# Kernel optimization log

Hardware: AMD Instinct MI355X
Metric: run time of the kernel (lower is better)

The kernel has to match this reference:

```python
import jax, jax.numpy as jnp
import numpy as np

EPS = 1e-12
LORA_RANK = 16

def setup_inputs() -> dict:
    key = jax.random.key(0)
    ks = jax.random.split(key, 7)
    bs, sq, din, dout = 8, 2048, 2048, 2048
    n_tasks, n_splits, n_skills, r = 32, 1, 8, LORA_RANK
    return {
        'x': jax.random.normal(ks[0], (bs, sq, din), dtype=jnp.float32),
        'W': jax.random.normal(ks[1], (dout, din), dtype=jnp.float32) * (1.0 / np.sqrt(din)),
        'b': jax.random.normal(ks[2], (dout,), dtype=jnp.float32) * 0.02,
        'module_logits': jax.random.normal(ks[3], (n_tasks, n_splits * n_skills), dtype=jnp.float32) * 0.001,
        'A': jax.random.normal(ks[4], (n_splits, n_skills, din // n_splits, r), dtype=jnp.float32) * 0.02,
        'B': jax.random.normal(ks[5], (n_splits, n_skills, r, dout // n_splits), dtype=jnp.float32) * 0.02,
        'tasks': jax.random.randint(ks[6], (bs,), 0, n_tasks),
    }

def reference(x, W, b, module_logits, A, B, tasks):
    bs, sq, din = x.shape
    n_splits, n_skills, _, r = A.shape
    dout = W.shape[0]
    # Polytropon selector (eval mode): sigmoid + normalize over skills
    probs = jax.nn.sigmoid(module_logits[tasks]).reshape(bs, n_splits, n_skills)
    probs = probs / (probs.sum(-1, keepdims=True) + EPS)  # [bs, p, t]
    # WeightedSum combinor: per-example skill mixture of LoRA params
    A_c = jnp.einsum('bpt,ptir->bpir', probs, A)  # [bs, p, din/p, r]
    B_c = jnp.einsum('bpt,ptro->bpro', probs, B)  # [bs, p, r, dout/p]
    # LoRA forward: reshape to per-example [din, r] and [r, dout]
    A_r = A_c.reshape(bs, din, r)
    B_r = jnp.transpose(B_c, (0, 2, 1, 3)).reshape(bs, r, dout)
    lora = jnp.einsum('bsr,bro->bso', jnp.einsum('bsi,bir->bsr', x, A_r), B_r)
    base = jnp.einsum('bsi,oi->bso', x, W) + b
    return base + lora * (1.0 / r)
```

## Files before the change

### kernel.cpp

```cpp
#include <hip/hip_runtime.h>

typedef __attribute__((ext_vector_type(4))) float f32x4;
typedef __attribute__((ext_vector_type(8))) short bf16x8;

__device__ __forceinline__ unsigned short f2b(float f) {
  unsigned u = __float_as_uint(f);
  u = (u + 0x7FFFu + ((u >> 16) & 1u)) >> 16;
  return (unsigned short)u;
}

#define BAR() asm volatile("s_barrier" ::: "memory")
#define VMCNT(N) asm volatile("s_waitcnt vmcnt(" #N ")" ::: "memory")

__global__ void combine_kernel(const float* __restrict__ logits,
                               const int*   __restrict__ tasks,
                               const float* __restrict__ A,
                               const float* __restrict__ B,
                               unsigned short* __restrict__ Art,
                               unsigned short* __restrict__ Brt)
{
  int idx = blockIdx.x * 256 + threadIdx.x;
  int b = idx >> 11;
  int i = idx & 2047;
  if (b >= 8) return;
  int task = tasks[b];
  float p[8]; float s = 0.f;
  #pragma unroll
  for (int t = 0; t < 8; ++t) {
    float l = logits[task * 8 + t];
    float e = 1.f / (1.f + __expf(-l));
    p[t] = e; s += e;
  }
  float inv = 1.f / (s + 1e-12f);
  #pragma unroll
  for (int t = 0; t < 8; ++t) p[t] *= inv;

  float ar[16];
  #pragma unroll
  for (int r = 0; r < 16; ++r) ar[r] = 0.f;
  for (int t = 0; t < 8; ++t) {
    const float* ap = A + ((size_t)t * 2048 + i) * 16;
    float pt = p[t];
    #pragma unroll
    for (int r = 0; r < 16; ++r) ar[r] += pt * ap[r];
  }
  #pragma unroll
  for (int r = 0; r < 16; ++r)
    Art[((size_t)b * 16 + r) * 2048 + i] = f2b(ar[r]);

  float br[16];
  #pragma unroll
  for (int r = 0; r < 16; ++r) br[r] = 0.f;
  for (int t = 0; t < 8; ++t) {
    float pt = p[t];
    #pragma unroll
    for (int r = 0; r < 16; ++r) br[r] += pt * B[((size_t)t * 16 + r) * 2048 + i];
  }
  #pragma unroll
  for (int r = 0; r < 16; ++r)
    Brt[((size_t)b * 2048 + i) * 16 + r] = f2b(br[r] * 0.0625f);
}

__global__ void prep_kernel(const float* __restrict__ x,
                            const unsigned short* __restrict__ Art,
                            const float* __restrict__ W,
                            unsigned short* __restrict__ Wb,
                            unsigned short* __restrict__ xb,
                            unsigned short* __restrict__ xa)
{
  __shared__ float red[4][16][16];
  int blk = blockIdx.x;
  int tid = threadIdx.x;
  if (blk >= 1024) {
    int idx0 = (blk - 1024) * 256 + tid;
    #pragma unroll
    for (int c = 0; c < 32; ++c) {
      size_t i = ((size_t)idx0 + (size_t)c * 32768) * 4;
      f32x4 v = *(const f32x4*)(W + i);
      ushort4 o;
      o.x = f2b(v.x); o.y = f2b(v.y); o.z = f2b(v.z); o.w = f2b(v.w);
      *(ushort4*)(Wb + i) = o;
    }
    return;
  }
  int lane = tid & 63, wv = tid >> 6;
  int lr = lane & 15, hi = lane >> 4;
  int rowbase = blk * 16;
  int batch = rowbase >> 11;
  int row = rowbase + lr;
  f32x4 acc; acc.x = 0.f; acc.y = 0.f; acc.z = 0.f; acc.w = 0.f;
  const float* xrow = x + (size_t)row * 2048 + wv * 512 + hi * 8;
  unsigned short* xbrow = xb + (size_t)row * 2048 + wv * 512 + hi * 8;
  const unsigned short* artrow = Art + ((size_t)batch * 16 + lr) * 2048 + wv * 512 + hi * 8;
  #pragma unroll
  for (int ks = 0; ks < 16; ++ks) {
    f32x4 v0 = *(const f32x4*)(xrow + ks * 32);
    f32x4 v1 = *(const f32x4*)(xrow + ks * 32 + 4);
    bf16x8 av;
    av[0] = (short)f2b(v0.x); av[1] = (short)f2b(v0.y);
    av[2] = (short)f2b(v0.z); av[3] = (short)f2b(v0.w);
    av[4] = (short)f2b(v1.x); av[5] = (short)f2b(v1.y);
    av[6] = (short)f2b(v1.z); av[7] = (short)f2b(v1.w);
    *(bf16x8*)(xbrow + ks * 32) = av;
    bf16x8 bv = *(const bf16x8*)(artrow + ks * 32);
    acc = __builtin_amdgcn_mfma_f32_16x16x32_bf16(av, bv, acc, 0, 0, 0);
  }
  #pragma unroll
  for (int j = 0; j < 4; ++j) red[wv][hi * 4 + j][lr] = acc[j];
  __syncthreads();
  int rr = tid >> 4, cc = tid & 15;
  float s = red[0][rr][cc] + red[1][rr][cc] + red[2][rr][cc] + red[3][rr][cc];
  xa[(size_t)(rowbase + rr) * 16 + cc] = f2b(s);
}

__global__ __launch_bounds__(512)
void gemm_kernel(const unsigned short* __restrict__ xb,
                 const unsigned short* __restrict__ Wb,
                 const float* __restrict__ bias,
                 const unsigned short* __restrict__ xa,
                 const unsigned short* __restrict__ Brt,
                 float* __restrict__ out)
{
  __shared__ __align__(16) char lds[131072];
  const int tid = threadIdx.x;
  const int lane = tid & 63;
  const int wv = tid >> 6;
  const int wr = wv >> 2, wc = wv & 3;
  const int lr = lane & 15, hi = lane >> 4;
  const int hi16 = hi * 16;

  const int bid = blockIdx.x;
  const int swz = (bid & 7) * 64 + (bid >> 3);
  const int tm = swz >> 3, tn = swz & 7;
  const int rowbase = tm * 256, colbase = tn * 256;

  const int row0 = tid >> 3;
  const int cb0 = (tid & 7) * 16;
  const int scb_e = (cb0 ^ ((row0 & 7) << 4)) >> 1;
  const int rb5 = ((row0 >> 5) << 6) + (row0 & 31);

#define GL16(LDSOFF, GPTR) \
  __builtin_amdgcn_global_load_lds((const __attribute__((address_space(1))) unsigned int*)(GPTR), \
      (__attribute__((address_space(3))) unsigned int*)(lds + (LDSOFF)), 16, 0, 0)

#define STAGE_A(MH, DBUF, KOFF) { \
  const unsigned short* g_ = xb + (size_t)(rowbase + (MH)*64 + row0) * 2048 + (KOFF) + scb_e; \
  GL16((DBUF)*65536 + (MH)*16384 + tid*16, g_); \
  GL16((DBUF)*65536 + (MH)*16384 + 8192 + tid*16, g_ + 128*2048); \
}
#define STAGE_B(NH, DBUF, KOFF) { \
  const unsigned short* g_ = Wb + (size_t)(colbase + (NH)*32 + rb5) * 2048 + (KOFF) + scb_e; \
  GL16((DBUF)*65536 + 32768 + (NH)*16384 + tid*16, g_); \
  GL16((DBUF)*65536 + 32768 + (NH)*16384 + 8192 + tid*16, g_ + 128*2048); \
}

#define READ_A(MH, ABASE) \
  _Pragma("unroll") \
  for (int mf = 0; mf < 4; ++mf) { \
    int ar_ = (MH)*128 + wr*64 + mf*16 + lr; \
    _Pragma("unroll") \
    for (int kk = 0; kk < 2; ++kk) \
      a[mf][kk] = *(const bf16x8*)((ABASE) + ar_*128 + ((kk*64 + hi16) ^ ((ar_&7)<<4))); \
  }
#define READ_B(NH, BBASE, BREG) \
  _Pragma("unroll") \
  for (int nf = 0; nf < 2; ++nf) { \
    int br_ = (NH)*128 + wc*32 + nf*16 + lr; \
    _Pragma("unroll") \
    for (int kk = 0; kk < 2; ++kk) \
      BREG[nf][kk] = *(const bf16x8*)((BBASE) + br_*128 + ((kk*64 + hi16) ^ ((br_&7)<<4))); \
  }
#define MFMA_BLOCK(MH, NH, BREG) \
  __builtin_amdgcn_s_setprio(1); \
  _Pragma("unroll") \
  for (int mf = 0; mf < 4; ++mf) \
    _Pragma("unroll") \
    for (int nf = 0; nf < 2; ++nf) \
      _Pragma("unroll") \
      for (int kk = 0; kk < 2; ++kk) \
        acc[(MH)*4+mf][(NH)*2+nf] = __builtin_amdgcn_mfma_f32_16x16x32_bf16( \
            a[mf][kk], BREG[nf][kk], acc[(MH)*4+mf][(NH)*2+nf], 0, 0, 0); \
  __builtin_amdgcn_s_setprio(0);

  f32x4 acc[8][4];
  #pragma unroll
  for (int i = 0; i < 8; ++i)
    #pragma unroll
    for (int n = 0; n < 4; ++n) { acc[i][n].x = 0.f; acc[i][n].y = 0.f; acc[i][n].z = 0.f; acc[i][n].w = 0.f; }

  bf16x8 a[4][2], b0[2][2], b1[2][2];

  STAGE_A(0, 0, 0);
  STAGE_B(0, 0, 0);
  STAGE_A(1, 0, 0);
  STAGE_B(1, 0, 0);
  STAGE_A(0, 1, 64);
  STAGE_B(0, 1, 64);
  VMCNT(4);
  BAR();
  READ_A(0, lds);
  READ_B(0, lds + 32768, b0);

  for (int kt = 0; kt < 32; ++kt) {
    const int buf = kt & 1, nbuf = buf ^ 1;
    const char* Ab  = lds + buf * 65536;
    const char* Bb  = Ab + 32768;
    const char* Abn = lds + nbuf * 65536;
    const char* Bbn = Abn + 32768;
    const int k1 = (kt + 1) * 64, k2 = (kt + 2) * 64;

    BAR();
    READ_B(1, Bb, b1);
    if (kt < 31) STAGE_A(1, nbuf, k1);
    MFMA_BLOCK(0, 0, b0);

    BAR();
    if (kt < 31) STAGE_B(1, nbuf, k1);
    MFMA_BLOCK(0, 1, b1);
    READ_A(1, Ab);
    if (kt < 31) { VMCNT(4); }

    BAR();
    if (kt < 30) STAGE_A(0, buf, k2);
    MFMA_BLOCK(1, 0, b0);
    if (kt < 31) READ_B(0, Bbn, b0);

    BAR();
    if (kt < 30) STAGE_B(0, buf, k2);
    MFMA_BLOCK(1, 1, b1);
    if (kt < 31) READ_A(0, Abn);
    if (kt < 30) { VMCNT(4); }
    else if (kt == 30) { VMCNT(0); }
  }

  const int batch = rowbase >> 11;
  bf16x8 zf = (bf16x8)(short)0;
  bf16x8 ea[8], eb[4];
  #pragma unroll
  for (int i = 0; i < 8; ++i) {
    if (hi < 2)
      ea[i] = *(const bf16x8*)(xa + (size_t)(rowbase + wr * 128 + i * 16 + lr) * 16 + hi * 8);
    else
      ea[i] = zf;
  }
  #pragma unroll
  for (int n = 0; n < 4; ++n) {
    if (hi < 2)
      eb[n] = *(const bf16x8*)(Brt + ((size_t)batch * 2048 + colbase + wc * 64 + n * 16 + lr) * 16 + hi * 8);
    else
      eb[n] = zf;
  }
  #pragma unroll
  for (int i = 0; i < 8; ++i)
    #pragma unroll
    for (int n = 0; n < 4; ++n)
      acc[i][n] = __builtin_amdgcn_mfma_f32_16x16x32_bf16(ea[i], eb[n], acc[i][n], 0, 0, 0);

  #pragma unroll
  for (int n = 0; n < 4; ++n) {
    int col = colbase + wc * 64 + n * 16 + lr;
    float bbv = bias[col];
    #pragma unroll
    for (int i = 0; i < 8; ++i) {
      int r0 = rowbase + wr * 128 + i * 16 + hi * 4;
      #pragma unroll
      for (int j = 0; j < 4; ++j)
        out[(size_t)(r0 + j) * 2048 + col] = acc[i][n][j] + bbv;
    }
  }
#undef GL16
#undef STAGE_A
#undef STAGE_B
#undef READ_A
#undef READ_B
#undef MFMA_BLOCK
}

extern "C" void kernel_launch(void* const* d_in, const int* in_sizes, int n_in,
                              void* d_out, int out_size, void* d_ws, size_t ws_size,
                              hipStream_t stream) {
  const float* x      = (const float*)d_in[0];
  const float* W      = (const float*)d_in[1];
  const float* bias   = (const float*)d_in[2];
  const float* logits = (const float*)d_in[3];
  const float* A      = (const float*)d_in[4];
  const float* B      = (const float*)d_in[5];
  const int*   tasks  = (const int*)d_in[6];
  float* out = (float*)d_out;

  char* ws = (char*)d_ws;
  unsigned short* xb  = (unsigned short*)(ws);
  unsigned short* Wb  = (unsigned short*)(ws + 67108864);
  unsigned short* xa  = (unsigned short*)(ws + 67108864 + 8388608);
  unsigned short* Art = (unsigned short*)(ws + 67108864 + 8388608 + 524288);
  unsigned short* Brt = (unsigned short*)(ws + 67108864 + 8388608 + 1048576);

  combine_kernel<<<64, 256, 0, stream>>>(logits, tasks, A, B, Art, Brt);
  prep_kernel<<<1152, 256, 0, stream>>>(x, Art, W, Wb, xb, xa);
  gemm_kernel<<<512, 512, 0, stream>>>(xb, Wb, bias, xa, Brt, out);
}
```

Baseline: 191.9 us.

## Unroll GEMM main loop by two with register ping-pong and sched_group_barrier interleaving

```diff
diff --git a/kernel.cpp b/kernel.cpp
--- a/kernel.cpp
+++ b/kernel.cpp
@@ -11,6 +11,13 @@
 
 #define BAR() asm volatile("s_barrier" ::: "memory")
 #define VMCNT(N) asm volatile("s_waitcnt vmcnt(" #N ")" ::: "memory")
+#define LGKM0() { asm volatile("s_waitcnt lgkmcnt(0)" ::: "memory"); __builtin_amdgcn_sched_barrier(0); }
+#define SGB(m, n) __builtin_amdgcn_sched_group_barrier(m, n, 0)
+#define PAT_R4() { SGB(0x10,2); SGB(0x8,2);SGB(0x100,1); SGB(0x8,2);SGB(0x100,1); \
+                   SGB(0x8,2);SGB(0x100,1); SGB(0x8,2);SGB(0x100,1); SGB(0x8,8); }
+#define PAT_R8() { SGB(0x10,2); SGB(0x8,1);SGB(0x100,1); SGB(0x8,1);SGB(0x100,1); \
+                   SGB(0x8,1);SGB(0x100,1); SGB(0x8,1);SGB(0x100,1); SGB(0x8,1);SGB(0x100,1); \
+                   SGB(0x8,1);SGB(0x100,1); SGB(0x8,1);SGB(0x100,1); SGB(0x8,1);SGB(0x100,1); SGB(0x8,8); }
 
 __global__ void combine_kernel(const float* __restrict__ logits,
                                const int*   __restrict__ tasks,
@@ -154,23 +161,23 @@
   GL16((DBUF)*65536 + 32768 + (NH)*16384 + 8192 + tid*16, g_ + 128*2048); \
 }
 
-#define READ_A(MH, ABASE) \
+#define RD_A(MH, BUF, AV) \
   _Pragma("unroll") \
   for (int mf = 0; mf < 4; ++mf) { \
     int ar_ = (MH)*128 + wr*64 + mf*16 + lr; \
     _Pragma("unroll") \
     for (int kk = 0; kk < 2; ++kk) \
-      a[mf][kk] = *(const bf16x8*)((ABASE) + ar_*128 + ((kk*64 + hi16) ^ ((ar_&7)<<4))); \
-  }
-#define READ_B(NH, BBASE, BREG) \
+      AV[mf][kk] = *(const bf16x8*)(lds + (BUF)*65536 + ar_*128 + ((kk*64 + hi16) ^ ((ar_&7)<<4))); \
+  }
+#define RD_B(NH, BUF, BV) \
   _Pragma("unroll") \
   for (int nf = 0; nf < 2; ++nf) { \
     int br_ = (NH)*128 + wc*32 + nf*16 + lr; \
     _Pragma("unroll") \
     for (int kk = 0; kk < 2; ++kk) \
-      BREG[nf][kk] = *(const bf16x8*)((BBASE) + br_*128 + ((kk*64 + hi16) ^ ((br_&7)<<4))); \
-  }
-#define MFMA_BLOCK(MH, NH, BREG) \
+      BV[nf][kk] = *(const bf16x8*)(lds + (BUF)*65536 + 32768 + br_*128 + ((kk*64 + hi16) ^ ((br_&7)<<4))); \
+  }
+#define MM(MH, NH, AV, BV) \
   __builtin_amdgcn_s_setprio(1); \
   _Pragma("unroll") \
   for (int mf = 0; mf < 4; ++mf) \
@@ -179,16 +186,45 @@
       _Pragma("unroll") \
       for (int kk = 0; kk < 2; ++kk) \
         acc[(MH)*4+mf][(NH)*2+nf] = __builtin_amdgcn_mfma_f32_16x16x32_bf16( \
-            a[mf][kk], BREG[nf][kk], acc[(MH)*4+mf][(NH)*2+nf], 0, 0, 0); \
+            AV[mf][kk], BV[nf][kk], acc[(MH)*4+mf][(NH)*2+nf], 0, 0, 0); \
   __builtin_amdgcn_s_setprio(0);
 
+#define KTILE(B0C, B0N, BUFC, BUFN, KO1, KO2) { \
+   \
+  BAR(); LGKM0(); \
+  STAGE_A(1, BUFN, KO1); \
+  RD_B(1, BUFC, q); \
+  MM(0, 0, aE, B0C); \
+  PAT_R4(); \
+   \
+  BAR(); LGKM0(); \
+  STAGE_B(1, BUFN, KO1); \
+  RD_A(1, BUFC, aO); \
+  MM(0, 1, aE, q); \
+  PAT_R8(); \
+  VMCNT(4); \
+   \
+  BAR(); LGKM0(); \
+  STAGE_A(0, BUFC, KO2); \
+  RD_B(0, BUFN, B0N); \
+  MM(1, 0, aO, B0C); \
+  PAT_R4(); \
+   \
+  BAR(); LGKM0(); \
+  STAGE_B(0, BUFC, KO2); \
+  RD_A(0, BUFN, aE); \
+  MM(1, 1, aO, q); \
+  PAT_R8(); \
+  VMCNT(4); \
+}
+
   f32x4 acc[8][4];
   #pragma unroll
   for (int i = 0; i < 8; ++i)
     #pragma unroll
     for (int n = 0; n < 4; ++n) { acc[i][n].x = 0.f; acc[i][n].y = 0.f; acc[i][n].z = 0.f; acc[i][n].w = 0.f; }
 
-  bf16x8 a[4][2], b0[2][2], b1[2][2];
+  bf16x8 aE[4][2], aO[4][2], p0[2][2], p1[2][2], q[2][2];
 
   STAGE_A(0, 0, 0);
   STAGE_B(0, 0, 0);
@@ -198,40 +234,41 @@
   STAGE_B(0, 1, 64);
   VMCNT(4);
   BAR();
-  READ_A(0, lds);
-  READ_B(0, lds + 32768, b0);
-
-  for (int kt = 0; kt < 32; ++kt) {
-    const int buf = kt & 1, nbuf = buf ^ 1;
-    const char* Ab  = lds + buf * 65536;
-    const char* Bb  = Ab + 32768;
-    const char* Abn = lds + nbuf * 65536;
-    const char* Bbn = Abn + 32768;
-    const int k1 = (kt + 1) * 64, k2 = (kt + 2) * 64;
-
-    BAR();
-    READ_B(1, Bb, b1);
-    if (kt < 31) STAGE_A(1, nbuf, k1);
-    MFMA_BLOCK(0, 0, b0);
-
-    BAR();
-    if (kt < 31) STAGE_B(1, nbuf, k1);
-    MFMA_BLOCK(0, 1, b1);
-    READ_A(1, Ab);
-    if (kt < 31) { VMCNT(4); }
-
-    BAR();
-    if (kt < 30) STAGE_A(0, buf, k2);
-    MFMA_BLOCK(1, 0, b0);
-    if (kt < 31) READ_B(0, Bbn, b0);
-
-    BAR();
-    if (kt < 30) STAGE_B(0, buf, k2);
-    MFMA_BLOCK(1, 1, b1);
-    if (kt < 31) READ_A(0, Abn);
-    if (kt < 30) { VMCNT(4); }
-    else if (kt == 30) { VMCNT(0); }
-  }
+  RD_A(0, 0, aE);
+  RD_B(0, 0, p0);
+
+  for (int it = 0; it < 15; ++it) {
+    const int k1 = (2 * it + 1) * 64, k2 = (2 * it + 2) * 64, k3 = (2 * it + 3) * 64;
+    KTILE(p0, p1, 0, 1, k1, k2);
+    KTILE(p1, p0, 1, 0, k2, k3);
+  }
+
+  BAR(); LGKM0();
+  STAGE_A(1, 1, 31 * 64);
+  RD_B(1, 0, q);
+  MM(0, 0, aE, p0);
+  BAR(); LGKM0();
+  STAGE_B(1, 1, 31 * 64);
+  RD_A(1, 0, aO);
+  MM(0, 1, aE, q);
+  VMCNT(4);
+  BAR(); LGKM0();
+  RD_B(0, 1, p1);
+  MM(1, 0, aO, p0);
+  BAR(); LGKM0();
+  RD_A(0, 1, aE);
+  MM(1, 1, aO, q);
+  VMCNT(0);
+  BAR(); LGKM0();
+  RD_B(1, 1, q);
+  MM(0, 0, aE, p1);
+  BAR(); LGKM0();
+  RD_A(1, 1, aO);
+  MM(0, 1, aE, q);
+  BAR(); LGKM0();
+  MM(1, 0, aO, p1);
+  BAR(); LGKM0();
+  MM(1, 1, aO, q);
 
   const int batch = rowbase >> 11;
   bf16x8 zf = (bf16x8)(short)0;
@@ -271,9 +308,10 @@
 #undef GL16
 #undef STAGE_A
 #undef STAGE_B
-#undef READ_A
-#undef READ_B
-#undef MFMA_BLOCK
+#undef RD_A
+#undef RD_B
+#undef MM
+#undef KTILE
 }
 
 extern "C" void kernel_launch(void* const* d_in, const int* in_sizes, int n_in,
```

Measured after the change: 226.1 us. 17.9% more time.
